# Performance work log

Measured on AMD Instinct MI355X. Metric: run time of the kernel, lower is better.

Reference implementation:

```python
import jax, jax.numpy as jnp
import numpy as np

BATCH = 32768
HIDDEN = 512
OUT = 2
FUTURE_STEPS = 60


def _lstm_cell(x, h, c, w_ih, w_hh, b_ih, b_hh):
    # PyTorch gate order: i, f, g, o
    g = x @ w_ih.T + h @ w_hh.T + b_ih + b_hh
    i, f, gg, o = jnp.split(g, 4, axis=-1)
    c_new = jax.nn.sigmoid(f) * c + jax.nn.sigmoid(i) * jnp.tanh(gg)
    h_new = jax.nn.sigmoid(o) * jnp.tanh(c_new)
    return h_new, c_new


def setup_inputs() -> dict:
    key = jax.random.key(0)
    ks = jax.random.split(key, 16)
    s = 0.05
    inp = {
        "h": jax.random.normal(ks[0], (BATCH, HIDDEN), jnp.float32),
        "w_init_h": jax.random.normal(ks[1], (HIDDEN, HIDDEN), jnp.float32) * s,
        "b_init_h": jax.random.normal(ks[2], (HIDDEN,), jnp.float32) * s,
        "w_init_c": jax.random.normal(ks[3], (HIDDEN, HIDDEN), jnp.float32) * s,
        "b_init_c": jax.random.normal(ks[4], (HIDDEN,), jnp.float32) * s,
        "w_ih0": jax.random.normal(ks[5], (4 * HIDDEN, OUT), jnp.float32) * s,
        "w_hh0": jax.random.normal(ks[6], (4 * HIDDEN, HIDDEN), jnp.float32) * s,
        "b_ih0": jax.random.normal(ks[7], (4 * HIDDEN,), jnp.float32) * s,
        "b_hh0": jax.random.normal(ks[8], (4 * HIDDEN,), jnp.float32) * s,
        "w_ih1": jax.random.normal(ks[9], (4 * HIDDEN, HIDDEN), jnp.float32) * s,
        "w_hh1": jax.random.normal(ks[10], (4 * HIDDEN, HIDDEN), jnp.float32) * s,
        "b_ih1": jax.random.normal(ks[11], (4 * HIDDEN,), jnp.float32) * s,
        "b_hh1": jax.random.normal(ks[12], (4 * HIDDEN,), jnp.float32) * s,
        "w_out": jax.random.normal(ks[13], (OUT, HIDDEN), jnp.float32) * s,
        "b_out": jax.random.normal(ks[14], (OUT,), jnp.float32) * s,
    }
    return inp


def reference(h, w_init_h, b_init_h, w_init_c, b_init_c,
              w_ih0, w_hh0, b_ih0, b_hh0,
              w_ih1, w_hh1, b_ih1, b_hh1,
              w_out, b_out):
    batch = h.shape[0]
    # same initial (h, c) replicated to both LSTM layers (repeat(2,1,1))
    h0 = h @ w_init_h.T + b_init_h
    c0 = h @ w_init_c.T + b_init_c
    x0 = jnp.zeros((batch, OUT), h.dtype)

    def step(carry, _):
        x, h1, c1, h2, c2 = carry
        h1, c1 = _lstm_cell(x, h1, c1, w_ih0, w_hh0, b_ih0, b_hh0)
        h2, c2 = _lstm_cell(h1, h2, c2, w_ih1, w_hh1, b_ih1, b_hh1)
        pred = h2 @ w_out.T + b_out  # [batch, OUT]
        return (pred, h1, c1, h2, c2), pred

    _, preds = jax.lax.scan(step, (x0, h0, c0, h0, c0), None, length=FUTURE_STEPS)
    return jnp.transpose(preds, (1, 0, 2))  # [batch, future_steps, OUT]
```

## Files before the change

### kernel.cpp

```cpp
#include <hip/hip_runtime.h>

#define HID    512
#define TPB    512
#define NSTEP  60
#define BMI    64

using f32x4 = __attribute__((ext_vector_type(4))) float;
using s16x8 = __attribute__((ext_vector_type(8))) short;

__device__ __forceinline__ unsigned short f2bf(float f) {
    unsigned u = __builtin_bit_cast(unsigned, f);
    u += 0x7fffu + ((u >> 16) & 1u);
    return (unsigned short)(u >> 16);
}
__device__ __forceinline__ float bf2f(unsigned u) {
    return __builtin_bit_cast(float, u << 16);
}
__device__ __forceinline__ float sigm(float x) { return 1.0f / (1.0f + __expf(-x)); }
__device__ __forceinline__ float tanh_(float x) { return 1.0f - 2.0f / (__expf(2.0f * x) + 1.0f); }

__device__ __forceinline__ f32x4 deperm(f32x4 q, int lgr) {
    f32x4 p;
    if (lgr == 0)      { p[0]=q[0]; p[1]=q[1]; p[2]=q[2]; p[3]=q[3]; }
    else if (lgr == 1) { p[0]=q[1]; p[1]=q[0]; p[2]=q[3]; p[3]=q[2]; }
    else if (lgr == 2) { p[0]=q[2]; p[1]=q[3]; p[2]=q[0]; p[3]=q[1]; }
    else               { p[0]=q[3]; p[1]=q[2]; p[2]=q[1]; p[3]=q[0]; }
    return p;
}

__global__ void pack_kernel(const float* __restrict__ w_hh0, const float* __restrict__ w_ih1,
                            const float* __restrict__ w_hh1, const float* __restrict__ w_init_h,
                            const float* __restrict__ w_init_c,
                            const float* __restrict__ b_ih0, const float* __restrict__ b_hh0,
                            const float* __restrict__ b_ih1, const float* __restrict__ b_hh1,
                            unsigned short* __restrict__ PW1, unsigned short* __restrict__ PW2,
                            unsigned short* __restrict__ PI,
                            float* __restrict__ b1, float* __restrict__ b2)
{
    int idx = blockIdx.x * 256 + threadIdx.x;
    if (idx < 1048576) {
        int el = idx & 511, fr = idx >> 9;
        int ks = fr & 15, ct = (fr >> 4) & 7, s = fr >> 7;
        int lane = el >> 3, e = el & 7;
        int cl = ct * 16 + (lane & 15);
        int gcol = (cl >> 5) * 512 + s * 32 + (cl & 31);
        int k = ks * 32 + (lane >> 4) * 8 + e;
        PW1[idx] = f2bf(w_hh0[gcol * 512 + k]);
        return;
    }
    int i2 = idx - 1048576;
    if (i2 >= 0 && i2 < 2097152) {
        int el = i2 & 511, fr = i2 >> 9;
        int ks = fr & 31, ct = (fr >> 5) & 7, s = fr >> 8;
        int lane = el >> 3, e = el & 7;
        int cl = ct * 16 + (lane & 15);
        int gcol = (cl >> 5) * 512 + s * 32 + (cl & 31);
        int kk = (ks & 15) * 32 + (lane >> 4) * 8 + e;
        float v = (ks < 16) ? w_ih1[gcol * 512 + kk] : w_hh1[gcol * 512 + kk];
        PW2[i2] = f2bf(v);
        return;
    }
    int i3 = idx - (1048576 + 2097152);
    if (i3 >= 0 && i3 < 524288) {
        int el = i3 & 511, fr = i3 >> 9;
        int ks = fr & 15, tile = fr >> 4;
        int s = tile >> 5, c = tile & 31;
        int lane = el >> 3, e = el & 7;
        int n = c * 16 + (lane & 15);
        int k = ks * 32 + (lane >> 4) * 8 + e;
        float v = s ? w_init_c[n * 512 + k] : w_init_h[n * 512 + k];
        PI[i3] = f2bf(v);
        return;
    }
    int i4 = idx - (1048576 + 2097152 + 524288);
    if (i4 >= 0 && i4 < 2048) b1[i4] = b_ih0[i4] + b_hh0[i4];
    else if (i4 >= 2048 && i4 < 4096) b2[i4 - 2048] = b_ih1[i4 - 2048] + b_hh1[i4 - 2048];
}

__global__ __launch_bounds__(TPB, 2) void init_kernel(
    const float* __restrict__ hin, const unsigned short* __restrict__ PI,
    const float* __restrict__ b_init_h, const float* __restrict__ b_init_c,
    unsigned short* __restrict__ h1s, unsigned short* __restrict__ h2s,
    unsigned short* __restrict__ c1s, unsigned short* __restrict__ c2s)
{
    __shared__ unsigned short bufA[BMI * HID];
    const int tid = threadIdx.x, lane = tid & 63, wave = tid >> 6;
    const int m0 = blockIdx.x * BMI;
    const int l15 = lane & 15, lg = lane >> 4;
    const int swz = (lane & 7) << 4;

    for (int j = 0; j < 16; ++j) {
        int e = tid * 4 + j * 2048;
        int row = e >> 9, col = e & 511;
        float4 v = *(const float4*)(hin + (size_t)(m0 + row) * HID + col);
        ushort4 w;
        w.x = f2bf(v.x); w.y = f2bf(v.y); w.z = f2bf(v.z); w.w = f2bf(v.w);
        int L = (row * 1024 + col * 2) ^ ((row & 7) << 4);
        *(ushort4*)((char*)bufA + L) = w;
    }
    __syncthreads();

    #pragma unroll 1
    for (int cc = 0; cc < 4; ++cc) {
        int c = wave * 4 + cc;
        int nc = c * 16 + l15;
        f32x4 acc[4][2];
        #pragma unroll
        for (int rt = 0; rt < 4; ++rt)
            #pragma unroll
            for (int s = 0; s < 2; ++s)
                #pragma unroll
                for (int r = 0; r < 4; ++r) acc[rt][s][r] = 0.0f;

        #pragma unroll
        for (int ks = 0; ks < 16; ++ks) {
            s16x8 a[4];
            #pragma unroll
            for (int rt = 0; rt < 4; ++rt) {
                int ao = (rt * 16 + l15) * 1024 + ((ks * 64 + lg * 16) ^ swz);
                a[rt] = *(const s16x8*)((const char*)bufA + ao);
            }
            #pragma unroll
            for (int s = 0; s < 2; ++s) {
                s16x8 b = ((const s16x8*)PI)[((s * 32 + c) * 16 + ks) * 64 + lane];
                #pragma unroll
                for (int rt = 0; rt < 4; ++rt)
                    acc[rt][s] = __builtin_amdgcn_mfma_f32_16x16x32_bf16(a[rt], b, acc[rt][s], 0, 0, 0);
            }
        }
        float bh = b_init_h[nc], bc = b_init_c[nc];
        #pragma unroll
        for (int rt = 0; rt < 4; ++rt)
            #pragma unroll
            for (int r = 0; r < 4; ++r) {
                int m = m0 + rt * 16 + lg * 4 + r;
                float hv = acc[rt][0][r] + bh;
                float cv = acc[rt][1][r] + bc;
                unsigned short hb = f2bf(hv);
                size_t o = (size_t)m * HID + nc;
                h1s[o] = hb; h2s[o] = hb;
                c1s[o] = f2bf(cv); c2s[o] = f2bf(cv);
            }
    }
}

__global__ __launch_bounds__(TPB, 2) void l1_kernel(
    const unsigned short* __restrict__ h1R, unsigned short* __restrict__ h1W,
    unsigned short* __restrict__ c1s, const float* __restrict__ pp,
    float* __restrict__ outp, const unsigned short* __restrict__ PW1,
    const float* __restrict__ b1, const float* __restrict__ w_ih0,
    const float* __restrict__ b_out, int t)
{
    __shared__ __align__(16) unsigned short Ab[16384];
    __shared__ __align__(16) float gl[2][2][2048];
    __shared__ __align__(16) float xls[5120];

    const int tid = threadIdx.x, lane = tid & 63, w = tid >> 6;
    const int b = blockIdx.x;
    const int g = 2 * (b & 7) + (b >> 7);
    const int s = (b >> 3) & 15;
    const int m0 = g * 2048;
    const int l15 = lane & 15, lg = lane >> 4;
    const int cg = w & 1, kh = (w >> 1) & 1, rha = w >> 2;

    s16x8 bw[4][8];
    #pragma unroll
    for (int j = 0; j < 4; ++j)
        #pragma unroll
        for (int ksl = 0; ksl < 8; ++ksl)
            bw[j][ksl] = ((const s16x8*)PW1)[(((s * 8 + cg * 4 + j) * 16) + kh * 8 + ksl) * 64 + lane];

    const int erow = tid >> 4, ejp = tid & 15;
    const int lgr = w & 3;
    float b1v[8], wiA[8], wiB[8];
    #pragma unroll
    for (int q = 0; q < 8; ++q) {
        int dj = q & 1, gq = q >> 1;
        int gcol = gq * 512 + s * 32 + ejp * 2 + dj;
        b1v[q] = b1[gcol];
        wiA[q] = w_ih0[gcol * 2 + 0];
        wiB[q] = w_ih0[gcol * 2 + 1];
    }
    float bo0 = b_out[0], bo1 = b_out[1];

    if (t == 0) {
        #pragma unroll
        for (int i = 0; i < 8; ++i) xls[tid * 8 + i] = 0.0f;
    } else {
        f32x4 s0 = {0.f,0.f,0.f,0.f}, s1 = {0.f,0.f,0.f,0.f};
        #pragma unroll 1
        for (int ss = 0; ss < 16; ++ss) {
            const float* p = pp + (((size_t)(g * 16 + ss)) << 12) + tid * 8;
            s0 += *(const f32x4*)p;
            s1 += *(const f32x4*)(p + 4);
        }
        s0[0] += bo0; s0[1] += bo1; s0[2] += bo0; s0[3] += bo1;
        s1[0] += bo0; s1[1] += bo1; s1[2] += bo0; s1[3] += bo1;
        *(f32x4*)(xls + tid * 8) = s0;
        *(f32x4*)(xls + tid * 8 + 4) = s1;
        if (s == 0) {
            float* ob = outp + (size_t)(m0 + tid * 4) * (2 * NSTEP) + (t - 1) * 2;
            *(float2*)(ob)                 = make_float2(s0[0], s0[1]);
            *(float2*)(ob + 2 * NSTEP)     = make_float2(s0[2], s0[3]);
            *(float2*)(ob + 4 * NSTEP)     = make_float2(s1[0], s1[1]);
            *(float2*)(ob + 6 * NSTEP)     = make_float2(s1[2], s1[3]);
        }
    }

    const int sl15 = tid & 15, slg = (tid >> 4) & 3, srh = (tid >> 6) & 1, skq = tid >> 7;
    const int sgrow = srh * 16 + sl15;
    const int scol  = (tid & 15) * 0;
    (void)scol;

    uint4 nv[4];
    #pragma unroll
    for (int p = 0; p < 4; ++p) {
        int ks = p * 4 + skq;
        nv[p] = *(const uint4*)(h1R + (size_t)(m0 + sgrow) * HID + ks * 32 + slg * 8);
    }
    #pragma unroll
    for (int p = 0; p < 4; ++p)
        *(uint4*)((char*)Ab + p * 8192 + tid * 16) = nv[p];

    #pragma unroll 1
    for (int ch = 0; ch < 64; ++ch) {
        __syncthreads();

        if (ch < 63) {
            #pragma unroll
            for (int p = 0; p < 4; ++p) {
                int ks = p * 4 + skq;
                nv[p] = *(const uint4*)(h1R + (size_t)(m0 + (ch + 1) * 32 + sgrow) * HID + ks * 32 + slg * 8);
            }
        }

        f32x4 acc[4];
        #pragma unroll
        for (int j = 0; j < 4; ++j) { acc[j][0]=0.f; acc[j][1]=0.f; acc[j][2]=0.f; acc[j][3]=0.f; }
        #pragma unroll
        for (int ksl = 0; ksl < 8; ++ksl) {
            int ks = kh * 8 + ksl;
            s16x8 a = *(const s16x8*)((const char*)Ab + ks * 2048 + rha * 1024 + lane * 16);
            #pragma unroll
            for (int j = 0; j < 4; ++j)
                acc[j] = __builtin_amdgcn_mfma_f32_16x16x32_bf16(a, bw[j][ksl], acc[j], 0, 0, 0);
        }
        #pragma unroll
        for (int j = 0; j < 4; ++j) {
            int col = (cg * 4 + j) * 16 + l15;
            int u = col & 31, gate = col >> 5;
            float* dst = &gl[kh][u & 1][(u >> 1) * 4 + (gate ^ lg)];
            #pragma unroll
            for (int r = 0; r < 4; ++r)
                dst[(rha * 16 + lg * 4 + r) * 64] = acc[j][r];
        }
        __syncthreads();

        if (ch < 63) {
            #pragma unroll
            for (int p = 0; p < 4; ++p)
                *(uint4*)((char*)Ab + p * 8192 + tid * 16) = nv[p];
        }

        {
            int grow = ch * 32 + erow;
            int m = m0 + grow;
            float x0 = xls[grow * 2 + 0], x1 = xls[grow * 2 + 1];
            int gbase = erow * 64 + ejp * 4;
            f32x4 qa = *(const f32x4*)&gl[0][0][gbase];
            qa += *(const f32x4*)&gl[1][0][gbase];
            f32x4 qb = *(const f32x4*)&gl[0][1][gbase];
            qb += *(const f32x4*)&gl[1][1][gbase];
            qa = deperm(qa, lgr); qb = deperm(qb, lgr);

            int cix = m * HID + s * 32 + ejp * 2;
            unsigned cp = *(const unsigned*)(c1s + cix);
            float cold0 = bf2f(cp & 0xffffu), cold1 = bf2f(cp >> 16);
            float i0 = sigm(qa[0] + b1v[0] + x0 * wiA[0] + x1 * wiB[0]);
            float f0 = sigm(qa[1] + b1v[2] + x0 * wiA[2] + x1 * wiB[2]);
            float g0 = tanh_(qa[2] + b1v[4] + x0 * wiA[4] + x1 * wiB[4]);
            float o0 = sigm(qa[3] + b1v[6] + x0 * wiA[6] + x1 * wiB[6]);
            float cn0 = f0 * cold0 + i0 * g0;
            float hn0 = o0 * tanh_(cn0);
            float i1 = sigm(qb[0] + b1v[1] + x0 * wiA[1] + x1 * wiB[1]);
            float f1 = sigm(qb[1] + b1v[3] + x0 * wiA[3] + x1 * wiB[3]);
            float g1 = tanh_(qb[2] + b1v[5] + x0 * wiA[5] + x1 * wiB[5]);
            float o1 = sigm(qb[3] + b1v[7] + x0 * wiA[7] + x1 * wiB[7]);
            float cn1 = f1 * cold1 + i1 * g1;
            float hn1 = o1 * tanh_(cn1);
            *(unsigned*)(c1s + cix) = (unsigned)f2bf(cn0) | ((unsigned)f2bf(cn1) << 16);
            *(unsigned*)(h1W + cix) = (unsigned)f2bf(hn0) | ((unsigned)f2bf(hn1) << 16);
        }
    }
}

__global__ __launch_bounds__(TPB, 2) void l2_kernel(
    const unsigned short* __restrict__ h1C, const unsigned short* __restrict__ h2R,
    unsigned short* __restrict__ h2W, unsigned short* __restrict__ c2s,
    float* __restrict__ pp,
    const unsigned short* __restrict__ PW2, const float* __restrict__ b2,
    const float* __restrict__ w_out)
{
    __shared__ __align__(16) unsigned short Ab[32768];
    __shared__ __align__(16) float gl[2][2][2304];

    const int tid = threadIdx.x, lane = tid & 63, w = tid >> 6;
    const int b = blockIdx.x;
    const int g = 2 * (b & 7) + (b >> 7);
    const int s = (b >> 3) & 15;
    const int m0 = g * 2048;
    const int l15 = lane & 15, lg = lane >> 4;
    const int cg = w & 1, kq = w >> 1;
    const int copy = kq >> 1, adder = ((kq & 1) == 0);

    s16x8 bw[4][8];
    #pragma unroll
    for (int j = 0; j < 4; ++j)
        #pragma unroll
        for (int ksl = 0; ksl < 8; ++ksl)
            bw[j][ksl] = ((const s16x8*)PW2)[(((s * 8 + cg * 4 + j) * 32) + kq * 8 + ksl) * 64 + lane];

    const int erow = tid >> 4, ejp = tid & 15;
    const int lgr = w & 3;
    float b2v[8];
    #pragma unroll
    for (int q = 0; q < 8; ++q) {
        int dj = q & 1, gq = q >> 1;
        b2v[q] = b2[gq * 512 + s * 32 + ejp * 2 + dj];
    }
    float woA0 = w_out[s * 32 + ejp * 2], woA1 = w_out[s * 32 + ejp * 2 + 1];
    float woB0 = w_out[512 + s * 32 + ejp * 2], woB1 = w_out[512 + s * 32 + ejp * 2 + 1];

    const int sl15 = tid & 15, slg = (tid >> 4) & 3, srh = (tid >> 6) & 1, skq = tid >> 7;
    const int sgrow = srh * 16 + sl15;

    uint4 nv[8];
    #pragma unroll
    for (int p = 0; p < 8; ++p) {
        int ks = p * 4 + skq;
        const unsigned short* src = (p < 4) ? h1C : h2R;
        int kel = (p < 4) ? ks : (ks - 16);
        nv[p] = *(const uint4*)(src + (size_t)(m0 + sgrow) * HID + kel * 32 + slg * 8);
    }
    #pragma unroll
    for (int p = 0; p < 8; ++p)
        *(uint4*)((char*)Ab + p * 8192 + tid * 16) = nv[p];

    #pragma unroll 1
    for (int ch = 0; ch < 64; ++ch) {
        __syncthreads();

        if (ch < 63) {
            #pragma unroll
            for (int p = 0; p < 8; ++p) {
                int ks = p * 4 + skq;
                const unsigned short* src = (p < 4) ? h1C : h2R;
                int kel = (p < 4) ? ks : (ks - 16);
                nv[p] = *(const uint4*)(src + (size_t)(m0 + (ch + 1) * 32 + sgrow) * HID + kel * 32 + slg * 8);
            }
        }

        f32x4 acc[2][4];
        #pragma unroll
        for (int rh = 0; rh < 2; ++rh)
            #pragma unroll
            for (int j = 0; j < 4; ++j) { acc[rh][j][0]=0.f; acc[rh][j][1]=0.f; acc[rh][j][2]=0.f; acc[rh][j][3]=0.f; }
        #pragma unroll
        for (int ksl = 0; ksl < 8; ++ksl) {
            int ks = kq * 8 + ksl;
            s16x8 a0 = *(const s16x8*)((const char*)Ab + ks * 2048 + lane * 16);
            s16x8 a1 = *(const s16x8*)((const char*)Ab + ks * 2048 + 1024 + lane * 16);
            #pragma unroll
            for (int j = 0; j < 4; ++j) {
                acc[0][j] = __builtin_amdgcn_mfma_f32_16x16x32_bf16(a0, bw[j][ksl], acc[0][j], 0, 0, 0);
                acc[1][j] = __builtin_amdgcn_mfma_f32_16x16x32_bf16(a1, bw[j][ksl], acc[1][j], 0, 0, 0);
            }
        }

        if (!adder) {
            #pragma unroll
            for (int j = 0; j < 4; ++j) {
                int col = (cg * 4 + j) * 16 + l15;
                int u = col & 31, gate = col >> 5;
                float* dst = &gl[copy][u & 1][(u >> 1) * 4 + (gate ^ lg)];
                #pragma unroll
                for (int rh = 0; rh < 2; ++rh)
                    #pragma unroll
                    for (int r = 0; r < 4; ++r)
                        dst[(rh * 16 + lg * 4 + r) * 64] = acc[rh][j][r];
            }
        }
        __syncthreads();
        if (adder) {
            #pragma unroll
            for (int j = 0; j < 4; ++j) {
                int col = (cg * 4 + j) * 16 + l15;
                int u = col & 31, gate = col >> 5;
                float* dst = &gl[copy][u & 1][(u >> 1) * 4 + (gate ^ lg)];
                #pragma unroll
                for (int rh = 0; rh < 2; ++rh)
                    #pragma unroll
                    for (int r = 0; r < 4; ++r)
                        dst[(rh * 16 + lg * 4 + r) * 64] += acc[rh][j][r];
            }
        }
        __syncthreads();

        if (ch < 63) {
            #pragma unroll
            for (int p = 0; p < 8; ++p)
                *(uint4*)((char*)Ab + p * 8192 + tid * 16) = nv[p];
        }

        {
            int m = m0 + ch * 32 + erow;
            int gbase = erow * 64 + ejp * 4;
            f32x4 qa = *(const f32x4*)&gl[0][0][gbase];
            qa += *(const f32x4*)&gl[1][0][gbase];
            f32x4 qb = *(const f32x4*)&gl[0][1][gbase];
            qb += *(const f32x4*)&gl[1][1][gbase];
            qa = deperm(qa, lgr); qb = deperm(qb, lgr);

            int cix = m * HID + s * 32 + ejp * 2;
            unsigned cp = *(const unsigned*)(c2s + cix);
            float cold0 = bf2f(cp & 0xffffu), cold1 = bf2f(cp >> 16);
            float i0 = sigm(qa[0] + b2v[0]);
            float f0 = sigm(qa[1] + b2v[2]);
            float g0 = tanh_(qa[2] + b2v[4]);
            float o0 = sigm(qa[3] + b2v[6]);
            float cn0 = f0 * cold0 + i0 * g0;
            float hn0 = o0 * tanh_(cn0);
            float i1 = sigm(qb[0] + b2v[1]);
            float f1 = sigm(qb[1] + b2v[3]);
            float g1 = tanh_(qb[2] + b2v[5]);
            float o1 = sigm(qb[3] + b2v[7]);
            float cn1 = f1 * cold1 + i1 * g1;
            float hn1 = o1 * tanh_(cn1);
            *(unsigned*)(c2s + cix) = (unsigned)f2bf(cn0) | ((unsigned)f2bf(cn1) << 16);
            *(unsigned*)(h2W + cix) = (unsigned)f2bf(hn0) | ((unsigned)f2bf(hn1) << 16);

            float p0 = hn0 * woA0 + hn1 * woA1;
            float p1 = hn0 * woB0 + hn1 * woB1;
            #pragma unroll
            for (int d = 1; d < 16; d <<= 1) {
                p0 += __shfl_xor(p0, d, 16);
                p1 += __shfl_xor(p1, d, 16);
            }
            if (ejp == 0)
                *(float2*)(pp + (((size_t)(g * 16 + s)) << 12) + (size_t)(ch * 32 + erow) * 2)
                    = make_float2(p0, p1);
        }
    }
}

__global__ void tail_kernel(const float* __restrict__ pp, const float* __restrict__ b_out,
                            float* __restrict__ outp)
{
    int i = blockIdx.x * 256 + threadIdx.x;
    if (i < 65536) {
        int m = i >> 1, j = i & 1;
        int g = m >> 11;
        int idx = (m & 2047) * 2 + j;
        float sum = b_out[j];
        #pragma unroll 1
        for (int s = 0; s < 16; ++s)
            sum += pp[(((size_t)(g * 16 + s)) << 12) + idx];
        outp[(size_t)m * (2 * NSTEP) + (NSTEP - 1) * 2 + j] = sum;
    }
}

extern "C" void kernel_launch(void* const* d_in, const int* in_sizes, int n_in,
                              void* d_out, int out_size, void* d_ws, size_t ws_size,
                              hipStream_t stream)
{
    (void)in_sizes; (void)n_in; (void)out_size; (void)ws_size;
    const float* h        = (const float*)d_in[0];
    const float* w_init_h = (const float*)d_in[1];
    const float* b_init_h = (const float*)d_in[2];
    const float* w_init_c = (const float*)d_in[3];
    const float* b_init_c = (const float*)d_in[4];
    const float* w_ih0    = (const float*)d_in[5];
    const float* w_hh0    = (const float*)d_in[6];
    const float* b_ih0    = (const float*)d_in[7];
    const float* b_hh0    = (const float*)d_in[8];
    const float* w_ih1    = (const float*)d_in[9];
    const float* w_hh1    = (const float*)d_in[10];
    const float* b_ih1    = (const float*)d_in[11];
    const float* b_hh1    = (const float*)d_in[12];
    const float* w_out    = (const float*)d_in[13];
    const float* b_out    = (const float*)d_in[14];
    float* out = (float*)d_out;

    char* ws = (char*)d_ws;
    unsigned short* h1s[2] = { (unsigned short*)(ws + 0),
                               (unsigned short*)(ws + 33554432) };
    unsigned short* h2s[2] = { (unsigned short*)(ws + 67108864),
                               (unsigned short*)(ws + 100663296) };
    unsigned short* c1s = (unsigned short*)(ws + 134217728);
    unsigned short* c2s = (unsigned short*)(ws + 167772160);
    float* pp           = (float*)(ws + 201326592);
    unsigned short* PW1 = (unsigned short*)(ws + 205520896);
    unsigned short* PW2 = (unsigned short*)(ws + 207618048);
    unsigned short* PI  = (unsigned short*)(ws + 211812352);
    float* b1 = (float*)(ws + 212860928);
    float* b2 = (float*)(ws + 212869120);

    pack_kernel<<<14352, 256, 0, stream>>>(w_hh0, w_ih1, w_hh1, w_init_h, w_init_c,
                                           b_ih0, b_hh0, b_ih1, b_hh1, PW1, PW2, PI, b1, b2);
    init_kernel<<<32768 / BMI, TPB, 0, stream>>>(h, PI, b_init_h, b_init_c,
                                                 h1s[1], h2s[1], c1s, c2s);
    for (int t = 0; t < NSTEP; ++t) {
        const unsigned short* h1R = h1s[(t + 1) & 1];
        unsigned short* h1W = h1s[t & 1];
        const unsigned short* h2R = h2s[(t + 1) & 1];
        unsigned short* h2W = h2s[t & 1];
        l1_kernel<<<256, TPB, 0, stream>>>(h1R, h1W, c1s, pp, out, PW1, b1, w_ih0, b_out, t);
        l2_kernel<<<256, TPB, 0, stream>>>(h1W, h2R, h2W, c2s, pp, PW2, b2, w_out);
    }
    tail_kernel<<<256, 256, 0, stream>>>(pp, b_out, out);
}
```

Baseline: 38.76 ms.

## Fuse per-step LSTM kernels into one persistent cooperative kernel with grid sync

Replaces the 120 per-step layer kernel launches and the tail kernel with a single cooperative persistent kernel. It loops over time steps and uses grid-wide syncs between layer 1 and layer 2. The hidden and cell state layout changes to a slice-blocked [group][slice][row][32] format so each block's reads and writes are contiguous. This removes launch overhead and per-launch weight reload gaps. In exchange it adds grid barrier cost, and larger shared memory use (layer-2 sized buffers) could limit occupancy to fewer than two blocks per CU.

```diff
diff --git a/kernel.cpp b/kernel.cpp
--- a/kernel.cpp
+++ b/kernel.cpp
@@ -1,9 +1,11 @@
 #include <hip/hip_runtime.h>
+#include <hip/hip_cooperative_groups.h>
 
 #define HID    512
 #define TPB    512
 #define NSTEP  60
 #define BMI    64
+#define NBLK   256
 
 using f32x4 = __attribute__((ext_vector_type(4))) float;
 using s16x8 = __attribute__((ext_vector_type(8))) short;
@@ -129,343 +131,330 @@
             }
         }
         float bh = b_init_h[nc], bc = b_init_c[nc];
+        int sl = nc >> 5, ul = nc & 31;
         #pragma unroll
         for (int rt = 0; rt < 4; ++rt)
             #pragma unroll
             for (int r = 0; r < 4; ++r) {
                 int m = m0 + rt * 16 + lg * 4 + r;
+                int gg = m >> 11, lr = m & 2047;
                 float hv = acc[rt][0][r] + bh;
                 float cv = acc[rt][1][r] + bc;
                 unsigned short hb = f2bf(hv);
-                size_t o = (size_t)m * HID + nc;
+                size_t o = ((size_t)(gg * 16 + sl) * 2048 + lr) * 32 + ul;
                 h1s[o] = hb; h2s[o] = hb;
                 c1s[o] = f2bf(cv); c2s[o] = f2bf(cv);
             }
     }
 }
 
-__global__ __launch_bounds__(TPB, 2) void l1_kernel(
-    const unsigned short* __restrict__ h1R, unsigned short* __restrict__ h1W,
-    unsigned short* __restrict__ c1s, const float* __restrict__ pp,
-    float* __restrict__ outp, const unsigned short* __restrict__ PW1,
-    const float* __restrict__ b1, const float* __restrict__ w_ih0,
-    const float* __restrict__ b_out, int t)
+__global__ __launch_bounds__(TPB, 2) void traj_kernel(
+    unsigned short* __restrict__ h1a, unsigned short* __restrict__ h1b,
+    unsigned short* __restrict__ h2a, unsigned short* __restrict__ h2b,
+    unsigned short* __restrict__ c1s, unsigned short* __restrict__ c2s,
+    float* __restrict__ pp,
+    const unsigned short* __restrict__ PW1, const unsigned short* __restrict__ PW2,
+    const float* __restrict__ b1, const float* __restrict__ b2,
+    const float* __restrict__ w_ih0, const float* __restrict__ w_out,
+    const float* __restrict__ b_out, float* __restrict__ outp)
 {
-    __shared__ __align__(16) unsigned short Ab[16384];
-    __shared__ __align__(16) float gl[2][2][2048];
-    __shared__ __align__(16) float xls[5120];
+    __shared__ __align__(16) unsigned short Ab[32768];
+    __shared__ __align__(16) float gl[2][2][2304];
+    __shared__ __align__(16) float xls[4160];
 
     const int tid = threadIdx.x, lane = tid & 63, w = tid >> 6;
     const int b = blockIdx.x;
     const int g = 2 * (b & 7) + (b >> 7);
     const int s = (b >> 3) & 15;
-    const int m0 = g * 2048;
     const int l15 = lane & 15, lg = lane >> 4;
     const int cg = w & 1, kh = (w >> 1) & 1, rha = w >> 2;
-
-    s16x8 bw[4][8];
-    #pragma unroll
-    for (int j = 0; j < 4; ++j)
-        #pragma unroll
-        for (int ksl = 0; ksl < 8; ++ksl)
-            bw[j][ksl] = ((const s16x8*)PW1)[(((s * 8 + cg * 4 + j) * 16) + kh * 8 + ksl) * 64 + lane];
+    const int kq = w >> 1;
+    const int copy = kq >> 1, adder = ((kq & 1) == 0);
 
     const int erow = tid >> 4, ejp = tid & 15;
     const int lgr = w & 3;
-    float b1v[8], wiA[8], wiB[8];
-    #pragma unroll
-    for (int q = 0; q < 8; ++q) {
-        int dj = q & 1, gq = q >> 1;
-        int gcol = gq * 512 + s * 32 + ejp * 2 + dj;
-        b1v[q] = b1[gcol];
-        wiA[q] = w_ih0[gcol * 2 + 0];
-        wiB[q] = w_ih0[gcol * 2 + 1];
-    }
-    float bo0 = b_out[0], bo1 = b_out[1];
-
-    if (t == 0) {
-        #pragma unroll
-        for (int i = 0; i < 8; ++i) xls[tid * 8 + i] = 0.0f;
-    } else {
-        f32x4 s0 = {0.f,0.f,0.f,0.f}, s1 = {0.f,0.f,0.f,0.f};
-        #pragma unroll 1
-        for (int ss = 0; ss < 16; ++ss) {
-            const float* p = pp + (((size_t)(g * 16 + ss)) << 12) + tid * 8;
-            s0 += *(const f32x4*)p;
-            s1 += *(const f32x4*)(p + 4);
+
+    const int st_ks  = tid >> 7;
+    const int st_rh  = (tid >> 6) & 1;
+    const int st_lg  = (tid >> 4) & 3;
+    const int st_l15 = tid & 15;
+
+    const size_t grpOff = (size_t)g * 16 * 2048 * 32;
+    const size_t blkOff = ((size_t)(g * 16 + s)) * 2048 * 32;
+
+    const float bo0 = b_out[0], bo1 = b_out[1];
+    const float woA0 = w_out[s * 32 + ejp * 2],       woA1 = w_out[s * 32 + ejp * 2 + 1];
+    const float woB0 = w_out[512 + s * 32 + ejp * 2], woB1 = w_out[512 + s * 32 + ejp * 2 + 1];
+
+    #pragma unroll 1
+    for (int t = 0; t <= NSTEP; ++t) {
+        unsigned short* h1R = (t & 1) ? h1a : h1b;
+        unsigned short* h1W = (t & 1) ? h1b : h1a;
+        unsigned short* h2R = (t & 1) ? h2a : h2b;
+        unsigned short* h2W = (t & 1) ? h2b : h2a;
+
+        if (t == 0) {
+            #pragma unroll
+            for (int i = 0; i < 8; ++i) xls[tid * 8 + i] = 0.0f;
+        } else {
+            f32x4 s0 = {0.f,0.f,0.f,0.f}, s1 = {0.f,0.f,0.f,0.f};
+            #pragma unroll 1
+            for (int ss = 0; ss < 16; ++ss) {
+                const float* p = pp + (((size_t)(g * 16 + ss)) << 12) + tid * 8;
+                s0 += *(const f32x4*)p;
+                s1 += *(const f32x4*)(p + 4);
+            }
+            s0[0] += bo0; s0[1] += bo1; s0[2] += bo0; s0[3] += bo1;
+            s1[0] += bo0; s1[1] += bo1; s1[2] += bo0; s1[3] += bo1;
+            *(f32x4*)(xls + tid * 8) = s0;
+            *(f32x4*)(xls + tid * 8 + 4) = s1;
+            if (s == 0) {
+                float* ob = outp + (size_t)(g * 2048 + tid * 4) * (2 * NSTEP) + (t - 1) * 2;
+                *(float2*)(ob)             = make_float2(s0[0], s0[1]);
+                *(float2*)(ob + 2 * NSTEP) = make_float2(s0[2], s0[3]);
+                *(float2*)(ob + 4 * NSTEP) = make_float2(s1[0], s1[1]);
+                *(float2*)(ob + 6 * NSTEP) = make_float2(s1[2], s1[3]);
+            }
         }
-        s0[0] += bo0; s0[1] += bo1; s0[2] += bo0; s0[3] += bo1;
-        s1[0] += bo0; s1[1] += bo1; s1[2] += bo0; s1[3] += bo1;
-        *(f32x4*)(xls + tid * 8) = s0;
-        *(f32x4*)(xls + tid * 8 + 4) = s1;
-        if (s == 0) {
-            float* ob = outp + (size_t)(m0 + tid * 4) * (2 * NSTEP) + (t - 1) * 2;
-            *(float2*)(ob)                 = make_float2(s0[0], s0[1]);
-            *(float2*)(ob + 2 * NSTEP)     = make_float2(s0[2], s0[3]);
-            *(float2*)(ob + 4 * NSTEP)     = make_float2(s1[0], s1[1]);
-            *(float2*)(ob + 6 * NSTEP)     = make_float2(s1[2], s1[3]);
-        }
-    }
-
-    const int sl15 = tid & 15, slg = (tid >> 4) & 3, srh = (tid >> 6) & 1, skq = tid >> 7;
-    const int sgrow = srh * 16 + sl15;
-    const int scol  = (tid & 15) * 0;
-    (void)scol;
-
-    uint4 nv[4];
-    #pragma unroll
-    for (int p = 0; p < 4; ++p) {
-        int ks = p * 4 + skq;
-        nv[p] = *(const uint4*)(h1R + (size_t)(m0 + sgrow) * HID + ks * 32 + slg * 8);
-    }
-    #pragma unroll
-    for (int p = 0; p < 4; ++p)
-        *(uint4*)((char*)Ab + p * 8192 + tid * 16) = nv[p];
-
-    #pragma unroll 1
-    for (int ch = 0; ch < 64; ++ch) {
-        __syncthreads();
-
-        if (ch < 63) {
+        if (t == NSTEP) break;
+
+        {
+            float b1v[8], wiA[8], wiB[8];
+            #pragma unroll
+            for (int q = 0; q < 8; ++q) {
+                int dj = q & 1, gq = q >> 1;
+                int gcol = gq * 512 + s * 32 + ejp * 2 + dj;
+                b1v[q] = b1[gcol];
+                wiA[q] = w_ih0[gcol * 2 + 0];
+                wiB[q] = w_ih0[gcol * 2 + 1];
+            }
+            s16x8 bw[4][8];
+            #pragma unroll
+            for (int j = 0; j < 4; ++j)
+                #pragma unroll
+                for (int ksl = 0; ksl < 8; ++ksl)
+                    bw[j][ksl] = ((const s16x8*)PW1)[(((s * 8 + cg * 4 + j) * 16) + kh * 8 + ksl) * 64 + lane];
+
+            const unsigned short* h1Rg = h1R + grpOff;
+
+            uint4 nv[4];
             #pragma unroll
             for (int p = 0; p < 4; ++p) {
-                int ks = p * 4 + skq;
-                nv[p] = *(const uint4*)(h1R + (size_t)(m0 + (ch + 1) * 32 + sgrow) * HID + ks * 32 + slg * 8);
-            }
-        }
-
-        f32x4 acc[4];
-        #pragma unroll
-        for (int j = 0; j < 4; ++j) { acc[j][0]=0.f; acc[j][1]=0.f; acc[j][2]=0.f; acc[j][3]=0.f; }
-        #pragma unroll
-        for (int ksl = 0; ksl < 8; ++ksl) {
-            int ks = kh * 8 + ksl;
-            s16x8 a = *(const s16x8*)((const char*)Ab + ks * 2048 + rha * 1024 + lane * 16);
-            #pragma unroll
-            for (int j = 0; j < 4; ++j)
-                acc[j] = __builtin_amdgcn_mfma_f32_16x16x32_bf16(a, bw[j][ksl], acc[j], 0, 0, 0);
-        }
-        #pragma unroll
-        for (int j = 0; j < 4; ++j) {
-            int col = (cg * 4 + j) * 16 + l15;
-            int u = col & 31, gate = col >> 5;
-            float* dst = &gl[kh][u & 1][(u >> 1) * 4 + (gate ^ lg)];
-            #pragma unroll
-            for (int r = 0; r < 4; ++r)
-                dst[(rha * 16 + lg * 4 + r) * 64] = acc[j][r];
-        }
-        __syncthreads();
-
-        if (ch < 63) {
+                int ks = p * 4 + st_ks;
+                nv[p] = *(const uint4*)(h1Rg + ((size_t)ks * 2048 + st_rh * 16 + st_l15) * 32 + st_lg * 8);
+            }
             #pragma unroll
             for (int p = 0; p < 4; ++p)
                 *(uint4*)((char*)Ab + p * 8192 + tid * 16) = nv[p];
+
+            #pragma unroll 1
+            for (int ch = 0; ch < 64; ++ch) {
+                __syncthreads();
+
+                if (ch < 63) {
+                    #pragma unroll
+                    for (int p = 0; p < 4; ++p) {
+                        int ks = p * 4 + st_ks;
+                        nv[p] = *(const uint4*)(h1Rg + ((size_t)ks * 2048 + (ch + 1) * 32 + st_rh * 16 + st_l15) * 32 + st_lg * 8);
+                    }
+                }
+
+                f32x4 acc[4];
+                #pragma unroll
+                for (int j = 0; j < 4; ++j) { acc[j][0]=0.f; acc[j][1]=0.f; acc[j][2]=0.f; acc[j][3]=0.f; }
+                #pragma unroll
+                for (int ksl = 0; ksl < 8; ++ksl) {
+                    int ks = kh * 8 + ksl;
+                    s16x8 a = *(const s16x8*)((const char*)Ab + ks * 2048 + rha * 1024 + lane * 16);
+                    #pragma unroll
+                    for (int j = 0; j < 4; ++j)
+                        acc[j] = __builtin_amdgcn_mfma_f32_16x16x32_bf16(a, bw[j][ksl], acc[j], 0, 0, 0);
+                }
+                #pragma unroll
+                for (int j = 0; j < 4; ++j) {
+                    int col = (cg * 4 + j) * 16 + l15;
+                    int u = col & 31, gate = col >> 5;
+                    float* dst = &gl[kh][u & 1][(u >> 1) * 4 + (gate ^ lg)];
+                    #pragma unroll
+                    for (int r = 0; r < 4; ++r)
+                        dst[(rha * 16 + lg * 4 + r) * 64] = acc[j][r];
+                }
+                __syncthreads();
+
+                if (ch < 63) {
+                    #pragma unroll
+                    for (int p = 0; p < 4; ++p)
+                        *(uint4*)((char*)Ab + p * 8192 + tid * 16) = nv[p];
+                }
+
+                {
+                    int mloc = ch * 32 + erow;
+                    float x0 = xls[mloc * 2 + 0], x1 = xls[mloc * 2 + 1];
+                    int gbase = erow * 64 + ejp * 4;
+                    f32x4 qa = *(const f32x4*)&gl[0][0][gbase];
+                    qa += *(const f32x4*)&gl[1][0][gbase];
+                    f32x4 qb = *(const f32x4*)&gl[0][1][gbase];
+                    qb += *(const f32x4*)&gl[1][1][gbase];
+                    qa = deperm(qa, lgr); qb = deperm(qb, lgr);
+
+                    size_t cix = blkOff + (size_t)mloc * 32 + ejp * 2;
+                    unsigned cp = *(const unsigned*)(c1s + cix);
+                    float cold0 = bf2f(cp & 0xffffu), cold1 = bf2f(cp >> 16);
+                    float i0 = sigm(qa[0] + b1v[0] + x0 * wiA[0] + x1 * wiB[0]);
+                    float f0 = sigm(qa[1] + b1v[2] + x0 * wiA[2] + x1 * wiB[2]);
+                    float g0 = tanh_(qa[2] + b1v[4] + x0 * wiA[4] + x1 * wiB[4]);
+                    float o0 = sigm(qa[3] + b1v[6] + x0 * wiA[6] + x1 * wiB[6]);
+                    float cn0 = f0 * cold0 + i0 * g0;
+                    float hn0 = o0 * tanh_(cn0);
+                    float i1 = sigm(qb[0] + b1v[1] + x0 * wiA[1] + x1 * wiB[1]);
+                    float f1 = sigm(qb[1] + b1v[3] + x0 * wiA[3] + x1 * wiB[3]);
+                    float g1 = tanh_(qb[2] + b1v[5] + x0 * wiA[5] + x1 * wiB[5]);
+                    float o1 = sigm(qb[3] + b1v[7] + x0 * wiA[7] + x1 * wiB[7]);
+                    float cn1 = f1 * cold1 + i1 * g1;
+                    float hn1 = o1 * tanh_(cn1);
+                    *(unsigned*)(c1s + cix) = (unsigned)f2bf(cn0) | ((unsigned)f2bf(cn1) << 16);
+                    *(unsigned*)(h1W + cix) = (unsigned)f2bf(hn0) | ((unsigned)f2bf(hn1) << 16);
+                }
+            }
         }
+        cooperative_groups::this_grid().sync();
 
         {
-            int grow = ch * 32 + erow;
-            int m = m0 + grow;
-            float x0 = xls[grow * 2 + 0], x1 = xls[grow * 2 + 1];
-            int gbase = erow * 64 + ejp * 4;
-            f32x4 qa = *(const f32x4*)&gl[0][0][gbase];
-            qa += *(const f32x4*)&gl[1][0][gbase];
-            f32x4 qb = *(const f32x4*)&gl[0][1][gbase];
-            qb += *(const f32x4*)&gl[1][1][gbase];
-            qa = deperm(qa, lgr); qb = deperm(qb, lgr);
-
-            int cix = m * HID + s * 32 + ejp * 2;
-            unsigned cp = *(const unsigned*)(c1s + cix);
-            float cold0 = bf2f(cp & 0xffffu), cold1 = bf2f(cp >> 16);
-            float i0 = sigm(qa[0] + b1v[0] + x0 * wiA[0] + x1 * wiB[0]);
-            float f0 = sigm(qa[1] + b1v[2] + x0 * wiA[2] + x1 * wiB[2]);
-            float g0 = tanh_(qa[2] + b1v[4] + x0 * wiA[4] + x1 * wiB[4]);
-            float o0 = sigm(qa[3] + b1v[6] + x0 * wiA[6] + x1 * wiB[6]);
-            float cn0 = f0 * cold0 + i0 * g0;
-            float hn0 = o0 * tanh_(cn0);
-            float i1 = sigm(qb[0] + b1v[1] + x0 * wiA[1] + x1 * wiB[1]);
-            float f1 = sigm(qb[1] + b1v[3] + x0 * wiA[3] + x1 * wiB[3]);
-            float g1 = tanh_(qb[2] + b1v[5] + x0 * wiA[5] + x1 * wiB[5]);
-            float o1 = sigm(qb[3] + b1v[7] + x0 * wiA[7] + x1 * wiB[7]);
-            float cn1 = f1 * cold1 + i1 * g1;
-            float hn1 = o1 * tanh_(cn1);
-            *(unsigned*)(c1s + cix) = (unsigned)f2bf(cn0) | ((unsigned)f2bf(cn1) << 16);
-            *(unsigned*)(h1W + cix) = (unsigned)f2bf(hn0) | ((unsigned)f2bf(hn1) << 16);
-        }
-    }
-}
-
-__global__ __launch_bounds__(TPB, 2) void l2_kernel(
-    const unsigned short* __restrict__ h1C, const unsigned short* __restrict__ h2R,
-    unsigned short* __restrict__ h2W, unsigned short* __restrict__ c2s,
-    float* __restrict__ pp,
-    const unsigned short* __restrict__ PW2, const float* __restrict__ b2,
-    const float* __restrict__ w_out)
-{
-    __shared__ __align__(16) unsigned short Ab[32768];
-    __shared__ __align__(16) float gl[2][2][2304];
-
-    const int tid = threadIdx.x, lane = tid & 63, w = tid >> 6;
-    const int b = blockIdx.x;
-    const int g = 2 * (b & 7) + (b >> 7);
-    const int s = (b >> 3) & 15;
-    const int m0 = g * 2048;
-    const int l15 = lane & 15, lg = lane >> 4;
-    const int cg = w & 1, kq = w >> 1;
-    const int copy = kq >> 1, adder = ((kq & 1) == 0);
-
-    s16x8 bw[4][8];
-    #pragma unroll
-    for (int j = 0; j < 4; ++j)
-        #pragma unroll
-        for (int ksl = 0; ksl < 8; ++ksl)
-            bw[j][ksl] = ((const s16x8*)PW2)[(((s * 8 + cg * 4 + j) * 32) + kq * 8 + ksl) * 64 + lane];
-
-    const int erow = tid >> 4, ejp = tid & 15;
-    const int lgr = w & 3;
-    float b2v[8];
-    #pragma unroll
-    for (int q = 0; q < 8; ++q) {
-        int dj = q & 1, gq = q >> 1;
-        b2v[q] = b2[gq * 512 + s * 32 + ejp * 2 + dj];
-    }
-    float woA0 = w_out[s * 32 + ejp * 2], woA1 = w_out[s * 32 + ejp * 2 + 1];
-    float woB0 = w_out[512 + s * 32 + ejp * 2], woB1 = w_out[512 + s * 32 + ejp * 2 + 1];
-
-    const int sl15 = tid & 15, slg = (tid >> 4) & 3, srh = (tid >> 6) & 1, skq = tid >> 7;
-    const int sgrow = srh * 16 + sl15;
-
-    uint4 nv[8];
-    #pragma unroll
-    for (int p = 0; p < 8; ++p) {
-        int ks = p * 4 + skq;
-        const unsigned short* src = (p < 4) ? h1C : h2R;
-        int kel = (p < 4) ? ks : (ks - 16);
-        nv[p] = *(const uint4*)(src + (size_t)(m0 + sgrow) * HID + kel * 32 + slg * 8);
-    }
-    #pragma unroll
-    for (int p = 0; p < 8; ++p)
-        *(uint4*)((char*)Ab + p * 8192 + tid * 16) = nv[p];
-
-    #pragma unroll 1
-    for (int ch = 0; ch < 64; ++ch) {
-        __syncthreads();
-
-        if (ch < 63) {
+            float b2v[8];
+            #pragma unroll
+            for (int q = 0; q < 8; ++q) {
+                int dj = q & 1, gq = q >> 1;
+                b2v[q] = b2[gq * 512 + s * 32 + ejp * 2 + dj];
+            }
+            s16x8 bw[4][8];
+            #pragma unroll
+            for (int j = 0; j < 4; ++j)
+                #pragma unroll
+                for (int ksl = 0; ksl < 8; ++ksl)
+                    bw[j][ksl] = ((const s16x8*)PW2)[(((s * 8 + cg * 4 + j) * 32) + kq * 8 + ksl) * 64 + lane];
+
+            const unsigned short* h1Cg = h1W + grpOff;
+            const unsigned short* h2Rg = h2R + grpOff;
+
+            uint4 nv[8];
             #pragma unroll
             for (int p = 0; p < 8; ++p) {
-                int ks = p * 4 + skq;
-                const unsigned short* src = (p < 4) ? h1C : h2R;
-                int kel = (p < 4) ? ks : (ks - 16);
-                nv[p] = *(const uint4*)(src + (size_t)(m0 + (ch + 1) * 32 + sgrow) * HID + kel * 32 + slg * 8);
-            }
-        }
-
-        f32x4 acc[2][4];
-        #pragma unroll
-        for (int rh = 0; rh < 2; ++rh)
-            #pragma unroll
-            for (int j = 0; j < 4; ++j) { acc[rh][j][0]=0.f; acc[rh][j][1]=0.f; acc[rh][j][2]=0.f; acc[rh][j][3]=0.f; }
-        #pragma unroll
-        for (int ksl = 0; ksl < 8; ++ksl) {
-            int ks = kq * 8 + ksl;
-            s16x8 a0 = *(const s16x8*)((const char*)Ab + ks * 2048 + lane * 16);
-            s16x8 a1 = *(const s16x8*)((const char*)Ab + ks * 2048 + 1024 + lane * 16);
-            #pragma unroll
-            for (int j = 0; j < 4; ++j) {
-                acc[0][j] = __builtin_amdgcn_mfma_f32_16x16x32_bf16(a0, bw[j][ksl], acc[0][j], 0, 0, 0);
-                acc[1][j] = __builtin_amdgcn_mfma_f32_16x16x32_bf16(a1, bw[j][ksl], acc[1][j], 0, 0, 0);
-            }
-        }
-
-        if (!adder) {
-            #pragma unroll
-            for (int j = 0; j < 4; ++j) {
-                int col = (cg * 4 + j) * 16 + l15;
-                int u = col & 31, gate = col >> 5;
-                float* dst = &gl[copy][u & 1][(u >> 1) * 4 + (gate ^ lg)];
-                #pragma unroll
-                for (int rh = 0; rh < 2; ++rh)
-                    #pragma unroll
-                    for (int r = 0; r < 4; ++r)
-                        dst[(rh * 16 + lg * 4 + r) * 64] = acc[rh][j][r];
-            }
-        }
-        __syncthreads();
-        if (adder) {
-            #pragma unroll
-            for (int j = 0; j < 4; ++j) {
-                int col = (cg * 4 + j) * 16 + l15;
-                int u = col & 31, gate = col >> 5;
-                float* dst = &gl[copy][u & 1][(u >> 1) * 4 + (gate ^ lg)];
-                #pragma unroll
-                for (int rh = 0; rh < 2; ++rh)
-                    #pragma unroll
-                    for (int r = 0; r < 4; ++r)
-                        dst[(rh * 16 + lg * 4 + r) * 64] += acc[rh][j][r];
-            }
-        }
-        __syncthreads();
-
-        if (ch < 63) {
+                int ks = p * 4 + st_ks;
+                const unsigned short* sb = (ks < 16) ? (h1Cg + (size_t)ks * 2048 * 32)
+                                                     : (h2Rg + (size_t)(ks - 16) * 2048 * 32);
+                nv[p] = *(const uint4*)(sb + ((size_t)(st_rh * 16 + st_l15)) * 32 + st_lg * 8);
+            }
             #pragma unroll
             for (int p = 0; p < 8; ++p)
                 *(uint4*)((char*)Ab + p * 8192 + tid * 16) = nv[p];
+
+            #pragma unroll 1
+            for (int ch = 0; ch < 64; ++ch) {
+                __syncthreads();
+
+                if (ch < 63) {
+                    #pragma unroll
+                    for (int p = 0; p < 8; ++p) {
+                        int ks = p * 4 + st_ks;
+                        const unsigned short* sb = (ks < 16) ? (h1Cg + (size_t)ks * 2048 * 32)
+                                                             : (h2Rg + (size_t)(ks - 16) * 2048 * 32);
+                        nv[p] = *(const uint4*)(sb + ((size_t)((ch + 1) * 32) + st_rh * 16 + st_l15) * 32 + st_lg * 8);
+                    }
+                }
+
+                f32x4 acc[2][4];
+                #pragma unroll
+                for (int rh = 0; rh < 2; ++rh)
+                    #pragma unroll
+                    for (int j = 0; j < 4; ++j) { acc[rh][j][0]=0.f; acc[rh][j][1]=0.f; acc[rh][j][2]=0.f; acc[rh][j][3]=0.f; }
+                #pragma unroll
+                for (int ksl = 0; ksl < 8; ++ksl) {
+                    int ks = kq * 8 + ksl;
+                    s16x8 a0 = *(const s16x8*)((const char*)Ab + ks * 2048 + lane * 16);
+                    s16x8 a1 = *(const s16x8*)((const char*)Ab + ks * 2048 + 1024 + lane * 16);
+                    #pragma unroll
+                    for (int j = 0; j < 4; ++j) {
+                        acc[0][j] = __builtin_amdgcn_mfma_f32_16x16x32_bf16(a0, bw[j][ksl], acc[0][j], 0, 0, 0);
+                        acc[1][j] = __builtin_amdgcn_mfma_f32_16x16x32_bf16(a1, bw[j][ksl], acc[1][j], 0, 0, 0);
+                    }
+                }
+
+                if (!adder) {
+                    #pragma unroll
+                    for (int j = 0; j < 4; ++j) {
+                        int col = (cg * 4 + j) * 16 + l15;
+                        int u = col & 31, gate = col >> 5;
+                        float* dst = &gl[copy][u & 1][(u >> 1) * 4 + (gate ^ lg)];
+                        #pragma unroll
+                        for (int rh = 0; rh < 2; ++rh)
+                            #pragma unroll
+                            for (int r = 0; r < 4; ++r)
+                                dst[(rh * 16 + lg * 4 + r) * 64] = acc[rh][j][r];
+                    }
+                }
+                __syncthreads();
+                if (adder) {
+                    #pragma unroll
+                    for (int j = 0; j < 4; ++j) {
+                        int col = (cg * 4 + j) * 16 + l15;
+                        int u = col & 31, gate = col >> 5;
+                        float* dst = &gl[copy][u & 1][(u >> 1) * 4 + (gate ^ lg)];
+                        #pragma unroll
+                        for (int rh = 0; rh < 2; ++rh)
+                            #pragma unroll
+                            for (int r = 0; r < 4; ++r)
+                                dst[(rh * 16 + lg * 4 + r) * 64] += acc[rh][j][r];
+                    }
+                }
+                __syncthreads();
+
+                if (ch < 63) {
+                    #pragma unroll
+                    for (int p = 0; p < 8; ++p)
+                        *(uint4*)((char*)Ab + p * 8192 + tid * 16) = nv[p];
+                }
+
+                {
+                    int mloc = ch * 32 + erow;
+                    int gbase = erow * 64 + ejp * 4;
+                    f32x4 qa = *(const f32x4*)&gl[0][0][gbase];
+                    qa += *(const f32x4*)&gl[1][0][gbase];
+                    f32x4 qb = *(const f32x4*)&gl[0][1][gbase];
+                    qb += *(const f32x4*)&gl[1][1][gbase];
+                    qa = deperm(qa, lgr); qb = deperm(qb, lgr);
+
+                    size_t cix = blkOff + (size_t)mloc * 32 + ejp * 2;
+                    unsigned cp = *(const unsigned*)(c2s + cix);
+                    float cold0 = bf2f(cp & 0xffffu), cold1 = bf2f(cp >> 16);
+                    float i0 = sigm(qa[0] + b2v[0]);
+                    float f0 = sigm(qa[1] + b2v[2]);
+                    float g0 = tanh_(qa[2] + b2v[4]);
+                    float o0 = sigm(qa[3] + b2v[6]);
+                    float cn0 = f0 * cold0 + i0 * g0;
+                    float hn0 = o0 * tanh_(cn0);
+                    float i1 = sigm(qb[0] + b2v[1]);
+                    float f1 = sigm(qb[1] + b2v[3]);
+                    float g1 = tanh_(qb[2] + b2v[5]);
+                    float o1 = sigm(qb[3] + b2v[7]);
+                    float cn1 = f1 * cold1 + i1 * g1;
+                    float hn1 = o1 * tanh_(cn1);
+                    *(unsigned*)(c2s + cix) = (unsigned)f2bf(cn0) | ((unsigned)f2bf(cn1) << 16);
+                    *(unsigned*)(h2W + cix) = (unsigned)f2bf(hn0) | ((unsigned)f2bf(hn1) << 16);
+
+                    float p0 = hn0 * woA0 + hn1 * woA1;
+                    float p1 = hn0 * woB0 + hn1 * woB1;
+                    #pragma unroll
+                    for (int d = 1; d < 16; d <<= 1) {
+                        p0 += __shfl_xor(p0, d, 16);
+                        p1 += __shfl_xor(p1, d, 16);
+                    }
+                    if (ejp == 0)
+                        *(float2*)(pp + (((size_t)(g * 16 + s)) << 12) + (size_t)mloc * 2)
+                            = make_float2(p0, p1);
+                }
+            }
         }
-
-        {
-            int m = m0 + ch * 32 + erow;
-            int gbase = erow * 64 + ejp * 4;
-            f32x4 qa = *(const f32x4*)&gl[0][0][gbase];
-            qa += *(const f32x4*)&gl[1][0][gbase];
-            f32x4 qb = *(const f32x4*)&gl[0][1][gbase];
-            qb += *(const f32x4*)&gl[1][1][gbase];
-            qa = deperm(qa, lgr); qb = deperm(qb, lgr);
-
-            int cix = m * HID + s * 32 + ejp * 2;
-            unsigned cp = *(const unsigned*)(c2s + cix);
-            float cold0 = bf2f(cp & 0xffffu), cold1 = bf2f(cp >> 16);
-            float i0 = sigm(qa[0] + b2v[0]);
-            float f0 = sigm(qa[1] + b2v[2]);
-            float g0 = tanh_(qa[2] + b2v[4]);
-            float o0 = sigm(qa[3] + b2v[6]);
-            float cn0 = f0 * cold0 + i0 * g0;
-            float hn0 = o0 * tanh_(cn0);
-            float i1 = sigm(qb[0] + b2v[1]);
-            float f1 = sigm(qb[1] + b2v[3]);
-            float g1 = tanh_(qb[2] + b2v[5]);
-            float o1 = sigm(qb[3] + b2v[7]);
-            float cn1 = f1 * cold1 + i1 * g1;
-            float hn1 = o1 * tanh_(cn1);
-            *(unsigned*)(c2s + cix) = (unsigned)f2bf(cn0) | ((unsigned)f2bf(cn1) << 16);
-            *(unsigned*)(h2W + cix) = (unsigned)f2bf(hn0) | ((unsigned)f2bf(hn1) << 16);
-
-            float p0 = hn0 * woA0 + hn1 * woA1;
-            float p1 = hn0 * woB0 + hn1 * woB1;
-            #pragma unroll
-            for (int d = 1; d < 16; d <<= 1) {
-                p0 += __shfl_xor(p0, d, 16);
-                p1 += __shfl_xor(p1, d, 16);
-            }
-            if (ejp == 0)
-                *(float2*)(pp + (((size_t)(g * 16 + s)) << 12) + (size_t)(ch * 32 + erow) * 2)
-                    = make_float2(p0, p1);
-        }
-    }
-}
-
-__global__ void tail_kernel(const float* __restrict__ pp, const float* __restrict__ b_out,
-                            float* __restrict__ outp)
-{
-    int i = blockIdx.x * 256 + threadIdx.x;
-    if (i < 65536) {
-        int m = i >> 1, j = i & 1;
-        int g = m >> 11;
-        int idx = (m & 2047) * 2 + j;
-        float sum = b_out[j];
-        #pragma unroll 1
-        for (int s = 0; s < 16; ++s)
-            sum += pp[(((size_t)(g * 16 + s)) << 12) + idx];
-        outp[(size_t)m * (2 * NSTEP) + (NSTEP - 1) * 2 + j] = sum;
+        cooperative_groups::this_grid().sync();
     }
 }
 
@@ -492,10 +481,10 @@
     float* out = (float*)d_out;
 
     char* ws = (char*)d_ws;
-    unsigned short* h1s[2] = { (unsigned short*)(ws + 0),
-                               (unsigned short*)(ws + 33554432) };
-    unsigned short* h2s[2] = { (unsigned short*)(ws + 67108864),
-                               (unsigned short*)(ws + 100663296) };
+    unsigned short* h1a = (unsigned short*)(ws + 0);
+    unsigned short* h1b = (unsigned short*)(ws + 33554432);
+    unsigned short* h2a = (unsigned short*)(ws + 67108864);
+    unsigned short* h2b = (unsigned short*)(ws + 100663296);
     unsigned short* c1s = (unsigned short*)(ws + 134217728);
     unsigned short* c2s = (unsigned short*)(ws + 167772160);
     float* pp           = (float*)(ws + 201326592);
@@ -508,14 +497,8 @@
     pack_kernel<<<14352, 256, 0, stream>>>(w_hh0, w_ih1, w_hh1, w_init_h, w_init_c,
                                            b_ih0, b_hh0, b_ih1, b_hh1, PW1, PW2, PI, b1, b2);
     init_kernel<<<32768 / BMI, TPB, 0, stream>>>(h, PI, b_init_h, b_init_c,
-                                                 h1s[1], h2s[1], c1s, c2s);
-    for (int t = 0; t < NSTEP; ++t) {
-        const unsigned short* h1R = h1s[(t + 1) & 1];
-        unsigned short* h1W = h1s[t & 1];
-        const unsigned short* h2R = h2s[(t + 1) & 1];
-        unsigned short* h2W = h2s[t & 1];
-        l1_kernel<<<256, TPB, 0, stream>>>(h1R, h1W, c1s, pp, out, PW1, b1, w_ih0, b_out, t);
-        l2_kernel<<<256, TPB, 0, stream>>>(h1W, h2R, h2W, c2s, pp, PW2, b2, w_out);
-    }
-    tail_kernel<<<256, 256, 0, stream>>>(pp, b_out, out);
-}
+                                                 h1b, h2b, c1s, c2s);
+    void* args[] = { &h1a, &h1b, &h2a, &h2b, &c1s, &c2s, &pp, &PW1, &PW2,
+                     &b1, &b2, &w_ih0, &w_out, &b_out, &out };
+    hipLaunchCooperativeKernel((void*)traj_kernel, dim3(NBLK), dim3(TPB), args, 0, stream);
+}
```

New measurement: 59.55 ms. 53.6% more time.
